# Performance work log

Hardware: AMD Instinct MI355X
Metric: run time of the kernel (lower is better)

## Reference

```python
import jax, jax.numpy as jnp
import numpy as np

NUM_CLASSES = 9
B, H, W = 8, 768, 768


def setup_inputs() -> dict:
    key = jax.random.key(0)
    k1, k2 = jax.random.split(key)
    masks = jax.random.randint(k1, (B, H, W), 0, NUM_CLASSES, dtype=jnp.int32)
    outputs = jax.random.normal(k2, (B, NUM_CLASSES, H, W), dtype=jnp.float32)
    return {"masks": masks, "outputs": outputs}


def reference(masks, outputs):
    b, c, h, w = outputs.shape
    k = NUM_CLASSES
    eye = jnp.eye(k, dtype=outputs.dtype)
    smooth = eye * 0.9 + (1.0 - eye) * (0.1 / 8.0)  # [K, K] smoothed targets

    # Fused segment-mean over all pixels: segment id = batch*K + class label.
    feats = jnp.transpose(outputs, (0, 2, 3, 1)).reshape(b * h * w, c)  # [BHW, C]
    ids = (jnp.arange(b, dtype=jnp.int32)[:, None, None] * k + masks).reshape(-1)
    sums = jax.ops.segment_sum(feats, ids, num_segments=b * k).reshape(b, k, c)
    counts = jax.ops.segment_sum(
        jnp.ones((b * h * w,), outputs.dtype), ids, num_segments=b * k
    ).reshape(b, k)

    # torch.unique(mask)[1:] drops label 0 (background); mask absent classes.
    protos = sums[:, 1:, :] / jnp.maximum(counts[:, 1:, None], 1.0)  # [B, K-1, C]
    present = counts[:, 1:] > 0  # [B, K-1]

    logp = jax.nn.log_softmax(protos, axis=-1)  # [B, K-1, C]
    tgt = smooth[1:]  # [K-1, C] soft targets for classes 1..K-1
    per_proto = -jnp.sum(tgt[None, :, :] * logp, axis=-1)  # [B, K-1]

    n_present = jnp.maximum(jnp.sum(present).astype(outputs.dtype), 1.0)
    loss = jnp.sum(jnp.where(present, per_proto, 0.0)) / n_present
    return loss
```

## Files before the change

### kernel.cpp

```cpp
#include <hip/hip_runtime.h>
#include <hip/hip_bf16.h>
#include <math.h>

#define NB 8
#define NC 9
#define NK 9
#define PIXELS (768*768)
#define CHUNK 16384
#define CHUNKS_PER_PLANE (PIXELS / CHUNK)
#define BLOCK 256
#define PIX_PER_THREAD (CHUNK / BLOCK)

#define SUMS_ELEMS (NB * 8 * NC)
#define WS_FLOATS (SUMS_ELEMS + NB * 8)

__global__ __launch_bounds__(BLOCK)
void accum_kernel(const int* __restrict__ masks,
                  const float* __restrict__ outputs,
                  float* __restrict__ sums,
                  float* __restrict__ counts)
{
    int idx = blockIdx.x;
    int c = idx % NC;
    int gchunk = idx / NC;
    int chunk = gchunk % CHUNKS_PER_PLANE;
    int b = gchunk / CHUNKS_PER_PLANE;

    const float4* __restrict__ out4 =
        (const float4*)(outputs + ((size_t)(b * NC + c)) * PIXELS + (size_t)chunk * CHUNK);
    const int4* __restrict__ m4 =
        (const int4*)(masks + (size_t)b * PIXELS + (size_t)chunk * CHUNK);

    const bool do_count = (c == 0);

    float s[8];
    float cnt[8];
    #pragma unroll
    for (int k = 0; k < 8; ++k) { s[k] = 0.f; cnt[k] = 0.f; }

    int t = threadIdx.x;

    #pragma unroll 4
    for (int i = 0; i < PIX_PER_THREAD / 4; ++i) {
        float4 v = out4[t + i * BLOCK];
        int4   m = m4[t + i * BLOCK];
        #pragma unroll
        for (int k = 1; k <= 8; ++k) {
            float acc = s[k - 1];
            acc += (m.x == k) ? v.x : 0.f;
            acc += (m.y == k) ? v.y : 0.f;
            acc += (m.z == k) ? v.z : 0.f;
            acc += (m.w == k) ? v.w : 0.f;
            s[k - 1] = acc;
        }
        if (do_count) {
            #pragma unroll
            for (int k = 1; k <= 8; ++k) {
                float acc = cnt[k - 1];
                acc += (m.x == k) ? 1.f : 0.f;
                acc += (m.y == k) ? 1.f : 0.f;
                acc += (m.z == k) ? 1.f : 0.f;
                acc += (m.w == k) ? 1.f : 0.f;
                cnt[k - 1] = acc;
            }
        }
    }

    #pragma unroll
    for (int k = 0; k < 8; ++k) {
        float v = s[k];
        #pragma unroll
        for (int off = 32; off > 0; off >>= 1) v += __shfl_down(v, off, 64);
        s[k] = v;
        if (do_count) {
            float w = cnt[k];
            #pragma unroll
            for (int off = 32; off > 0; off >>= 1) w += __shfl_down(w, off, 64);
            cnt[k] = w;
        }
    }

    __shared__ float red_s[BLOCK / 64][8];
    __shared__ float red_c[BLOCK / 64][8];
    int wave = threadIdx.x >> 6;
    int lane = threadIdx.x & 63;
    if (lane == 0) {
        #pragma unroll
        for (int k = 0; k < 8; ++k) { red_s[wave][k] = s[k]; red_c[wave][k] = cnt[k]; }
    }
    __syncthreads();

    if (threadIdx.x < 8) {
        float tot = 0.f, totc = 0.f;
        #pragma unroll
        for (int w = 0; w < BLOCK / 64; ++w) { tot += red_s[w][threadIdx.x]; totc += red_c[w][threadIdx.x]; }
        atomicAdd(&sums[(b * 8 + threadIdx.x) * NC + c], tot);
        if (do_count) atomicAdd(&counts[b * 8 + threadIdx.x], totc);
    }
}

__global__ __launch_bounds__(64)
void finalize_kernel(const float* __restrict__ sums,
                     const float* __restrict__ counts,
                     float* __restrict__ out)
{
    int t = threadIdx.x;
    int b = t >> 3;
    int cls = t & 7;

    float cntv = counts[b * 8 + cls];
    float denom = fmaxf(cntv, 1.0f);

    float p[NC];
    float mx = -INFINITY;
    #pragma unroll
    for (int c = 0; c < NC; ++c) {
        p[c] = sums[(b * 8 + cls) * NC + c] / denom;
        mx = fmaxf(mx, p[c]);
    }
    float se = 0.f;
    #pragma unroll
    for (int c = 0; c < NC; ++c) se += expf(p[c] - mx);
    float lse = logf(se);

    float per = 0.f;
    #pragma unroll
    for (int c = 0; c < NC; ++c) {
        float tgt = (c == cls + 1) ? 0.9f : 0.0125f;
        per -= tgt * (p[c] - mx - lse);
    }

    bool present = cntv > 0.f;
    float val = present ? per : 0.f;
    float np  = present ? 1.f : 0.f;
    #pragma unroll
    for (int off = 32; off > 0; off >>= 1) {
        val += __shfl_down(val, off, 64);
        np  += __shfl_down(np,  off, 64);
    }
    if (t == 0) out[0] = val / fmaxf(np, 1.f);
}

extern "C" void kernel_launch(void* const* d_in, const int* in_sizes, int n_in,
                              void* d_out, int out_size, void* d_ws, size_t ws_size,
                              hipStream_t stream) {
    const int*   masks   = (const int*)d_in[0];
    const float* outputs = (const float*)d_in[1];
    float* sums   = (float*)d_ws;
    float* counts = sums + SUMS_ELEMS;

    hipMemsetAsync(d_ws, 0, WS_FLOATS * sizeof(float), stream);

    int grid = NB * CHUNKS_PER_PLANE * NC;
    accum_kernel<<<grid, BLOCK, 0, stream>>>(masks, outputs, sums, counts);
    finalize_kernel<<<1, 64, 0, stream>>>(sums, counts, (float*)d_out);
}
```

Measured before the change: 267.1 us.

## Process all channels per block reusing register-cached mask tile

Each block now loads its mask chunk once into registers and loops over all 9 channels, rather than launching a separate block per channel that re-reads the mask. This removes the repeated mask traffic, which was comparable in size to the feature traffic. The cost is a much smaller grid (fewer blocks) with more serial work per thread, plus more registers and shared memory per block. That may reduce latency hiding.

```diff
diff --git a/kernel.cpp b/kernel.cpp
--- a/kernel.cpp
+++ b/kernel.cpp
@@ -4,12 +4,12 @@
 
 #define NB 8
 #define NC 9
-#define NK 9
 #define PIXELS (768*768)
-#define CHUNK 16384
-#define CHUNKS_PER_PLANE (PIXELS / CHUNK)
 #define BLOCK 256
-#define PIX_PER_THREAD (CHUNK / BLOCK)
+#define PPT 24
+#define CHUNK_PX (BLOCK * PPT)
+#define NCHUNK (PIXELS / CHUNK_PX)
+#define NITER (PPT / 4)
 
 #define SUMS_ELEMS (NB * 8 * NC)
 #define WS_FLOATS (SUMS_ELEMS + NB * 8)
@@ -20,82 +20,93 @@
                   float* __restrict__ sums,
                   float* __restrict__ counts)
 {
-    int idx = blockIdx.x;
-    int c = idx % NC;
-    int gchunk = idx / NC;
-    int chunk = gchunk % CHUNKS_PER_PLANE;
-    int b = gchunk / CHUNKS_PER_PLANE;
+    int blk = blockIdx.x;
+    int chunk = blk % NCHUNK;
+    int b = blk / NCHUNK;
+    int t = threadIdx.x;
+    int wave = t >> 6;
+    int lane = t & 63;
 
-    const float4* __restrict__ out4 =
-        (const float4*)(outputs + ((size_t)(b * NC + c)) * PIXELS + (size_t)chunk * CHUNK);
     const int4* __restrict__ m4 =
-        (const int4*)(masks + (size_t)b * PIXELS + (size_t)chunk * CHUNK);
+        (const int4*)(masks + (size_t)b * PIXELS + (size_t)chunk * CHUNK_PX);
+    int4 m[NITER];
+    #pragma unroll
+    for (int i = 0; i < NITER; ++i) m[i] = m4[t + i * BLOCK];
 
-    const bool do_count = (c == 0);
+    __shared__ float red[NC][BLOCK / 64][8];
+    __shared__ float red_c[BLOCK / 64][8];
 
-    float s[8];
-    float cnt[8];
-    #pragma unroll
-    for (int k = 0; k < 8; ++k) { s[k] = 0.f; cnt[k] = 0.f; }
-
-    int t = threadIdx.x;
-
-    #pragma unroll 4
-    for (int i = 0; i < PIX_PER_THREAD / 4; ++i) {
-        float4 v = out4[t + i * BLOCK];
-        int4   m = m4[t + i * BLOCK];
+    {
+        float cnt[8];
         #pragma unroll
-        for (int k = 1; k <= 8; ++k) {
-            float acc = s[k - 1];
-            acc += (m.x == k) ? v.x : 0.f;
-            acc += (m.y == k) ? v.y : 0.f;
-            acc += (m.z == k) ? v.z : 0.f;
-            acc += (m.w == k) ? v.w : 0.f;
-            s[k - 1] = acc;
-        }
-        if (do_count) {
+        for (int k = 0; k < 8; ++k) cnt[k] = 0.f;
+        #pragma unroll
+        for (int i = 0; i < NITER; ++i) {
             #pragma unroll
             for (int k = 1; k <= 8; ++k) {
-                float acc = cnt[k - 1];
-                acc += (m.x == k) ? 1.f : 0.f;
-                acc += (m.y == k) ? 1.f : 0.f;
-                acc += (m.z == k) ? 1.f : 0.f;
-                acc += (m.w == k) ? 1.f : 0.f;
-                cnt[k - 1] = acc;
+                float a = cnt[k - 1];
+                a += (m[i].x == k) ? 1.f : 0.f;
+                a += (m[i].y == k) ? 1.f : 0.f;
+                a += (m[i].z == k) ? 1.f : 0.f;
+                a += (m[i].w == k) ? 1.f : 0.f;
+                cnt[k - 1] = a;
             }
+        }
+        #pragma unroll
+        for (int k = 0; k < 8; ++k) {
+            float v = cnt[k];
+            #pragma unroll
+            for (int off = 32; off > 0; off >>= 1) v += __shfl_down(v, off, 64);
+            if (lane == 0) red_c[wave][k] = v;
         }
     }
 
-    #pragma unroll
-    for (int k = 0; k < 8; ++k) {
-        float v = s[k];
+    for (int c = 0; c < NC; ++c) {
+        const float4* __restrict__ o4 =
+            (const float4*)(outputs + ((size_t)(b * NC + c)) * PIXELS
+                            + (size_t)chunk * CHUNK_PX);
+        float s[8];
         #pragma unroll
-        for (int off = 32; off > 0; off >>= 1) v += __shfl_down(v, off, 64);
-        s[k] = v;
-        if (do_count) {
-            float w = cnt[k];
+        for (int k = 0; k < 8; ++k) s[k] = 0.f;
+
+        #pragma unroll
+        for (int i = 0; i < NITER; ++i) {
+            float4 v = o4[t + i * BLOCK];
             #pragma unroll
-            for (int off = 32; off > 0; off >>= 1) w += __shfl_down(w, off, 64);
-            cnt[k] = w;
+            for (int k = 1; k <= 8; ++k) {
+                float a = s[k - 1];
+                a += (m[i].x == k) ? v.x : 0.f;
+                a += (m[i].y == k) ? v.y : 0.f;
+                a += (m[i].z == k) ? v.z : 0.f;
+                a += (m[i].w == k) ? v.w : 0.f;
+                s[k - 1] = a;
+            }
+        }
+
+        #pragma unroll
+        for (int k = 0; k < 8; ++k) {
+            float v = s[k];
+            #pragma unroll
+            for (int off = 32; off > 0; off >>= 1) v += __shfl_down(v, off, 64);
+            if (lane == 0) red[c][wave][k] = v;
         }
     }
 
-    __shared__ float red_s[BLOCK / 64][8];
-    __shared__ float red_c[BLOCK / 64][8];
-    int wave = threadIdx.x >> 6;
-    int lane = threadIdx.x & 63;
-    if (lane == 0) {
-        #pragma unroll
-        for (int k = 0; k < 8; ++k) { red_s[wave][k] = s[k]; red_c[wave][k] = cnt[k]; }
-    }
     __syncthreads();
 
-    if (threadIdx.x < 8) {
-        float tot = 0.f, totc = 0.f;
+    if (t < NC * 8) {
+        int c = t >> 3;
+        int k = t & 7;
+        float tot = 0.f;
         #pragma unroll
-        for (int w = 0; w < BLOCK / 64; ++w) { tot += red_s[w][threadIdx.x]; totc += red_c[w][threadIdx.x]; }
-        atomicAdd(&sums[(b * 8 + threadIdx.x) * NC + c], tot);
-        if (do_count) atomicAdd(&counts[b * 8 + threadIdx.x], totc);
+        for (int w = 0; w < BLOCK / 64; ++w) tot += red[c][w][k];
+        atomicAdd(&sums[(b * 8 + k) * NC + c], tot);
+    } else if (t < NC * 8 + 8) {
+        int k = t - NC * 8;
+        float tot = 0.f;
+        #pragma unroll
+        for (int w = 0; w < BLOCK / 64; ++w) tot += red_c[w][k];
+        atomicAdd(&counts[b * 8 + k], tot);
     }
 }
 
@@ -151,7 +162,7 @@
 
     hipMemsetAsync(d_ws, 0, WS_FLOATS * sizeof(float), stream);
 
-    int grid = NB * CHUNKS_PER_PLANE * NC;
+    int grid = NB * NCHUNK;
     accum_kernel<<<grid, BLOCK, 0, stream>>>(masks, outputs, sums, counts);
     finalize_kernel<<<1, 64, 0, stream>>>(sums, counts, (float*)d_out);
 }
```

Result: faster. 259.0 us (-3.0%).
